# Kernel tuning notes

Hardware: AMD Instinct MI355X
Metric: run time of the kernel (lower is better)

## Reference

```python
import jax, jax.numpy as jnp
import numpy as np

BLOCK_SIZE = 64
SPARSITY_RATIO = 0.5


def _band_mask(seq_len, block_size, sparsity_ratio):
    # Block (i, j) is computed iff max(0, i-w) <= j < min(nb, i+w), w = int(nb*ratio).
    nb = seq_len // block_size
    w = int(nb * sparsity_ratio)
    ib = jnp.arange(nb)
    bm = (ib[None, :] >= ib[:, None] - w) & (ib[None, :] < ib[:, None] + w)  # [nb, nb]
    return jnp.repeat(jnp.repeat(bm, block_size, axis=0), block_size, axis=1)  # [S, S]


def setup_inputs() -> dict:
    key = jax.random.key(0)
    kq, kk, kv = jax.random.split(key, 3)
    B, S, D = 4, 4096, 128
    return {
        "query": jax.random.normal(kq, (B, S, D), dtype=jnp.float32),
        "key": jax.random.normal(kk, (B, S, D), dtype=jnp.float32),
        "value": jax.random.normal(kv, (B, S, D), dtype=jnp.float32),
    }


def reference(query, key, value):
    B, S, D = query.shape
    mask = _band_mask(S, BLOCK_SIZE, SPARSITY_RATIO)  # [S, S] bool
    scores = jnp.einsum('bqd,bkd->bqk', query, key)  # [B, S, S]
    # Outside-band entries stay exactly 0 (NOT -inf) — matches torch.zeros init.
    scores = jnp.where(mask[None, :, :], scores, jnp.zeros((), scores.dtype))
    probs = jax.nn.softmax(scores, axis=-1)
    return jnp.matmul(probs, value)  # [B, S, D]
```

## Files before the change

### kernel.cpp

```cpp
#include <hip/hip_runtime.h>


typedef _Float16 f16;
typedef __attribute__((ext_vector_type(8))) _Float16 f16x8;
typedef __attribute__((ext_vector_type(4))) _Float16 f16x4;
typedef __attribute__((ext_vector_type(4))) float f32x4;
typedef __attribute__((ext_vector_type(8))) short short8;
typedef __attribute__((ext_vector_type(4))) unsigned short u16x4;
typedef __attribute__((ext_vector_type(8))) unsigned short u16x8;

#define MFMA16(a, b, c) __builtin_amdgcn_mfma_f32_16x16x32_f16((a), (b), (c), 0, 0, 0)
#define MFMABF(a, b, c) __builtin_amdgcn_mfma_f32_16x16x32_bf16((a), (b), (c), 0, 0, 0)

#define BATCH 4
#define SEQ   4096
#define DIM   128
#define NB    64
#define WBAND 32
#define LOG2E 1.44269504088896f
#define TSTR  72

#define TILE  16384
#define CHUNKS 8
#define PART_STRIDE 16896

#define KA_OFF 0
#define KB_OFF 16384
#define VA_OFF 32768
#define VB_OFF 49152

#define WAIT0 asm volatile("s_waitcnt vmcnt(0)" ::: "memory")

__device__ __forceinline__ void gl16(const char* g, char* l) {
  __builtin_amdgcn_global_load_lds(
      (const __attribute__((address_space(1))) void*)g,
      (__attribute__((address_space(3))) void*)l, 16, 0, 0);
}

__device__ __forceinline__ unsigned int pk_bf16(float a, float b) {
  unsigned int r;
  asm("v_cvt_pk_bf16_f32 %0, %1, %2" : "=v"(r) : "v"(a), "v"(b));
  return r;
}

__device__ __forceinline__ unsigned short f2bf(float x) {
  unsigned int u = __float_as_uint(x);
  u += 0x7FFFu + ((u >> 16) & 1u);
  return (unsigned short)(u >> 16);
}

__global__ __launch_bounds__(256) void convert_kernel(
    const float* __restrict__ K, const float* __restrict__ V,
    f16* __restrict__ KF, unsigned short* __restrict__ VF,
    float* __restrict__ BS) {
  __shared__ unsigned short T[128 * TSTR];
  const int blk = blockIdx.x;
  const int b = blk >> 6, jb = blk & 63;
  const int s0 = jb * 64;
  const int t = threadIdx.x;

#pragma unroll
  for (int i = 0; i < 8; ++i) {
    int idx = t + i * 256;
    int row = idx >> 5;
    int c4 = (idx & 31) * 4;
    float4 v = *(const float4*)(V + (size_t)(b * SEQ + s0 + row) * DIM + c4);
    T[(c4 + 0) * TSTR + row] = f2bf(v.x);
    T[(c4 + 1) * TSTR + row] = f2bf(v.y);
    T[(c4 + 2) * TSTR + row] = f2bf(v.z);
    T[(c4 + 3) * TSTR + row] = f2bf(v.w);
  }

  char* kt = (char*)KF + (size_t)blk * TILE;
#pragma unroll
  for (int i = 0; i < 4; ++i) {
    int idx = t + i * 256;
    int frag = idx >> 6, lane = idx & 63;
    int ks = frag >> 2, jt = frag & 3;
    int row = jt * 16 + (lane & 15);
    int d0 = ks * 32 + (lane >> 4) * 8;
    const float* src = K + ((size_t)(b * SEQ + s0 + row)) * DIM + d0;
    float4 a = *(const float4*)src;
    float4 d = *(const float4*)(src + 4);
    f16x8 h = {(f16)a.x, (f16)a.y, (f16)a.z, (f16)a.w,
               (f16)d.x, (f16)d.y, (f16)d.z, (f16)d.w};
    *(f16x8*)(kt + idx * 16) = h;
  }
  __syncthreads();

  char* vt = (char*)VF + (size_t)blk * TILE;
#pragma unroll
  for (int i = 0; i < 4; ++i) {
    int idx = t + i * 256;
    int frag = idx >> 6, lane = idx & 63;
    int ks2 = frag >> 3, nt = frag & 7;
    int d = nt * 16 + (lane & 15);
    int k0 = ks2 * 32 + ((lane >> 4) & 3) * 4;
    u16x4 x = *(const u16x4*)(T + d * TSTR + k0);
    u16x4 y = *(const u16x4*)(T + d * TSTR + k0 + 16);
    u16x8 h = {x[0], x[1], x[2], x[3], y[0], y[1], y[2], y[3]};
    *(u16x8*)(vt + idx * 16) = h;
  }

  if (t < 128) {
    float s = 0.f;
    for (int k = 0; k < 64; ++k)
      s += __uint_as_float(((unsigned int)T[t * TSTR + k]) << 16);
    BS[(b * NB + jb) * DIM + t] = s;
  }
}

__global__ __launch_bounds__(256, 2) void attn_kernel(
    const float* __restrict__ Q, const f16* __restrict__ KF,
    const unsigned short* __restrict__ VF, char* __restrict__ PART) {
  __shared__ __align__(16) char smem[65536];

  const int id = blockIdx.x;
  const int lin = (id & 7) * 128 + (id >> 3);
  const int ck = lin & 7;
  const int pair = lin >> 3;
  const int b = pair >> 5, p = pair & 31;

  const int t = threadIdx.x;
  const int w = t >> 6, l = t & 63, lg = l >> 4, ll = l & 15;
  const int half = w >> 1, qh = w & 1;
  const int myib = p * 2 + half;

  const int jloU = max(0, p * 2 - WBAND);
  const int jhiU = min(NB, p * 2 + 1 + WBAND);
  const int lenU = jhiU - jloU;
  const int base = lenU >> 3, rem = lenU & 7;
  const int j0 = jloU + ck * base + min(ck, rem);
  const int nloc = base + (ck < rem ? 1 : 0);
  const int mylo = max(0, myib - WBAND);
  const int myhi = min(NB, myib + WBAND);

  f16x8 qf[2][4];
#pragma unroll
  for (int s = 0; s < 2; ++s) {
    const float* qrow =
        Q + ((size_t)(b * SEQ + myib * 64 + qh * 32 + s * 16 + ll)) * DIM;
#pragma unroll
    for (int ks = 0; ks < 4; ++ks) {
      int d0 = ks * 32 + lg * 8;
      float4 a = *(const float4*)(qrow + d0);
      float4 cc = *(const float4*)(qrow + d0 + 4);
      float vv[8] = {a.x, a.y, a.z, a.w, cc.x, cc.y, cc.z, cc.w};
#pragma unroll
      for (int e = 0; e < 8; ++e) qf[s][ks][e] = (f16)(vv[e] * LOG2E);
    }
  }

  float ell[2] = {0.f, 0.f};
  f32x4 o[2][8];
#pragma unroll
  for (int s = 0; s < 2; ++s)
#pragma unroll
    for (int nt = 0; nt < 8; ++nt) o[s][nt] = (f32x4){0.f, 0.f, 0.f, 0.f};

  auto stage_group = [&](int g) {
    const int jA = j0 + 2 * g;
    {
      const char* kg = (const char*)KF + ((size_t)(b * NB + jA)) * TILE + t * 16;
      const char* vg = (const char*)VF + ((size_t)(b * NB + jA)) * TILE + t * 16;
#pragma unroll
      for (int i = 0; i < 4; ++i) gl16(kg + i * 4096, smem + KA_OFF + t * 16 + i * 4096);
#pragma unroll
      for (int i = 0; i < 4; ++i) gl16(vg + i * 4096, smem + VA_OFF + t * 16 + i * 4096);
    }
    if (2 * g + 1 < nloc) {
      const int jB = jA + 1;
      const char* kg = (const char*)KF + ((size_t)(b * NB + jB)) * TILE + t * 16;
      const char* vg = (const char*)VF + ((size_t)(b * NB + jB)) * TILE + t * 16;
#pragma unroll
      for (int i = 0; i < 4; ++i) gl16(kg + i * 4096, smem + KB_OFF + t * 16 + i * 4096);
#pragma unroll
      for (int i = 0; i < 4; ++i) gl16(vg + i * 4096, smem + VB_OFF + t * 16 + i * 4096);
    }
  };

  auto compute = [&](int j, const char* kb, const char* vb) {
    if (j < mylo || j >= myhi) return;

    f32x4 sacc[2][4];
#pragma unroll
    for (int s = 0; s < 2; ++s)
#pragma unroll
      for (int jt = 0; jt < 4; ++jt) sacc[s][jt] = (f32x4){0.f, 0.f, 0.f, 0.f};

    __builtin_amdgcn_s_setprio(1);
#pragma unroll
    for (int ks = 0; ks < 4; ++ks) {
#pragma unroll
      for (int jt = 0; jt < 4; ++jt) {
        f16x8 kf = *(const f16x8*)(kb + (ks * 4 + jt) * 1024 + l * 16);
        sacc[0][jt] = MFMA16(kf, qf[0][ks], sacc[0][jt]);
        sacc[1][jt] = MFMA16(kf, qf[1][ks], sacc[1][jt]);
      }
    }
    __builtin_amdgcn_s_setprio(0);

    short8 pa[2][2];
#pragma unroll
    for (int s = 0; s < 2; ++s) {
      float rsum = 0.f;
#pragma unroll
      for (int ks2 = 0; ks2 < 2; ++ks2) {
        float pe[8];
#pragma unroll
        for (int u = 0; u < 2; ++u)
#pragma unroll
          for (int r = 0; r < 4; ++r) {
            float p = __builtin_amdgcn_exp2f(sacc[s][ks2 * 2 + u][r]);
            rsum += p;
            pe[u * 4 + r] = p;
          }
        union { unsigned int w[4]; short8 v; } pk;
#pragma unroll
        for (int h2 = 0; h2 < 4; ++h2)
          pk.w[h2] = pk_bf16(pe[h2 * 2], pe[h2 * 2 + 1]);
        pa[s][ks2] = pk.v;
      }
      ell[s] += rsum;
    }

    __builtin_amdgcn_s_setprio(1);
#pragma unroll
    for (int ks2 = 0; ks2 < 2; ++ks2) {
#pragma unroll
      for (int nt = 0; nt < 8; ++nt) {
        short8 vbf = *(const short8*)(vb + (ks2 * 8 + nt) * 1024 + l * 16);
        o[0][nt] = MFMABF(pa[0][ks2], vbf, o[0][nt]);
        o[1][nt] = MFMABF(pa[1][ks2], vbf, o[1][nt]);
      }
    }
    __builtin_amdgcn_s_setprio(0);
  };

  const int ng = (nloc + 1) >> 1;
  stage_group(0);
  for (int g = 0; g < ng; ++g) {
    WAIT0;
    __syncthreads();

    compute(j0 + 2 * g, smem + KA_OFF, smem + VA_OFF);
    if (2 * g + 1 < nloc)
      compute(j0 + 2 * g + 1, smem + KB_OFF, smem + VB_OFF);

    __syncthreads();
    if (g + 1 < ng) stage_group(g + 1);
  }

#pragma unroll
  for (int s = 0; s < 2; ++s) {
    ell[s] += __shfl_xor(ell[s], 16);
    ell[s] += __shfl_xor(ell[s], 32);
  }

  float sb[2][4];
#pragma unroll
  for (int s = 0; s < 2; ++s) {
    float rinv = 1.f / ell[s];
#pragma unroll
    for (int r = 0; r < 4; ++r) sb[s][r] = __shfl(rinv, lg * 4 + r);
  }

  char* pb = PART + ((size_t)((pair * CHUNKS + ck) * 2 + half)) * PART_STRIDE;
#pragma unroll
  for (int s = 0; s < 2; ++s)
#pragma unroll
    for (int g = 0; g < 4; ++g) {
      f16x8 hh;
#pragma unroll
      for (int r = 0; r < 4; ++r) {
        hh[r] = (f16)(o[s][2 * g][r] * sb[s][r]);
        hh[4 + r] = (f16)(o[s][2 * g + 1][r] * sb[s][r]);
      }
      *(f16x8*)(pb + qh * 8192 + ((s * 4 + g) * 64 + l) * 16) = hh;
    }
  if (lg == 0) {
#pragma unroll
    for (int s = 0; s < 2; ++s)
      *(float2*)(pb + 16384 + (qh * 32 + s * 16 + ll) * 8) =
          make_float2(0.f, ell[s]);
  }
}

__global__ __launch_bounds__(256) void merge_kernel(
    const char* __restrict__ PART, const float* __restrict__ BS,
    float* __restrict__ Out) {
  __shared__ float VoutS[DIM];
  __shared__ float mlS[CHUNKS][64][2];

  const int id = blockIdx.x;
  const int lin = (id & 7) * 32 + (id >> 3);
  const int pair = lin >> 1, half = lin & 1;
  const int b = pair >> 5;
  const int ib = (pair & 31) * 2 + half;
  const int t = threadIdx.x;
  const int l = t & 63, lg = (t >> 4) & 3, ll = t & 15;
  const int sub = (t >> 6) & 1, qh = t >> 7;

  const int jlo = max(0, ib - WBAND);
  const int jhi = min(NB, ib + WBAND);
  const float cnt_out = (float)(SEQ - (jhi - jlo) * 64);

  if (t < DIM) {
    float s = 0.f;
    for (int j = 0; j < jlo; ++j) s += BS[(b * NB + j) * DIM + t];
    for (int j = jhi; j < NB; ++j) s += BS[(b * NB + j) * DIM + t];
    VoutS[t] = s;
  }

  const size_t pb0 = ((size_t)(pair * CHUNKS * 2 + half)) * PART_STRIDE;
  for (int i = t; i < CHUNKS * 64; i += 256) {
    int k = i >> 6, row = i & 63;
    *(float2*)&mlS[k][row][0] = *(const float2*)(
        PART + pb0 + (size_t)k * 2 * PART_STRIDE + 16384 + row * 8);
  }
  __syncthreads();

  float aw[4][CHUNKS], inv[4];
#pragma unroll
  for (int r = 0; r < 4; ++r) {
    int row = qh * 32 + sub * 16 + lg * 4 + r;
    float den = cnt_out;
#pragma unroll
    for (int k = 0; k < CHUNKS; ++k) {
      aw[r][k] = mlS[k][row][1];
      den += aw[r][k];
    }
    inv[r] = 1.f / den;
  }

  float acc[8][4];
#pragma unroll
  for (int nt = 0; nt < 8; ++nt)
#pragma unroll
    for (int r = 0; r < 4; ++r) acc[nt][r] = 0.f;

  for (int k = 0; k < CHUNKS; ++k) {
    const char* oc = PART + pb0 + (size_t)k * 2 * PART_STRIDE + qh * 8192;
#pragma unroll
    for (int g = 0; g < 4; ++g) {
      f16x8 h = *(const f16x8*)(oc + ((sub * 4 + g) * 64 + l) * 16);
#pragma unroll
      for (int r = 0; r < 4; ++r) {
        acc[2 * g][r] += aw[r][k] * (float)h[r];
        acc[2 * g + 1][r] += aw[r][k] * (float)h[4 + r];
      }
    }
  }

  const int q0 = ib * 64;
#pragma unroll
  for (int nt = 0; nt < 8; ++nt) {
    int col = nt * 16 + ll;
    float vout = VoutS[col];
#pragma unroll
    for (int r = 0; r < 4; ++r) {
      int row = qh * 32 + sub * 16 + lg * 4 + r;
      Out[((size_t)(b * SEQ + q0 + row)) * DIM + col] =
          (acc[nt][r] + vout) * inv[r];
    }
  }
}

extern "C" void kernel_launch(void* const* d_in, const int* in_sizes, int n_in,
                              void* d_out, int out_size, void* d_ws, size_t ws_size,
                              hipStream_t stream) {
  const float* Q = (const float*)d_in[0];
  const float* K = (const float*)d_in[1];
  const float* V = (const float*)d_in[2];
  float* Out = (float*)d_out;

  char* ws = (char*)d_ws;
  f16* KF = (f16*)ws;
  unsigned short* VF = (unsigned short*)(ws + (size_t)BATCH * NB * TILE);
  float* BS = (float*)(ws + 2 * (size_t)BATCH * NB * TILE);
  char* PART = ws + 2 * (size_t)BATCH * NB * TILE + (size_t)BATCH * NB * DIM * 4;

  convert_kernel<<<dim3(BATCH * NB), 256, 0, stream>>>(K, V, KF, VF, BS);
  attn_kernel<<<dim3(BATCH * NB / 2 * CHUNKS), 256, 0, stream>>>(Q, KF, VF, PART);
  merge_kernel<<<dim3(BATCH * NB), 256, 0, stream>>>(PART, BS, Out);
}
```

Baseline: 58.82 us.

## Load V fragments directly from global into registers, stage only K in LDS

Shrinks shared memory from 64KB to 16KB by staging only one K tile per iteration in LDS. V fragments are loaded straight from global memory into registers at the start of each compute step, so their latency overlaps the QK MFMAs and softmax. The two-tile grouped pipeline is replaced by a single-tile loop with two barriers per tile and no overlap of the K load with compute. The goal is higher occupancy and less LDS traffic, at the cost of more registers, exposed K-load latency and more frequent synchronisation.

```diff
diff --git a/kernel.cpp b/kernel.cpp
--- a/kernel.cpp
+++ b/kernel.cpp
@@ -23,13 +23,6 @@
 #define TILE  16384
 #define CHUNKS 8
 #define PART_STRIDE 16896
-
-#define KA_OFF 0
-#define KB_OFF 16384
-#define VA_OFF 32768
-#define VB_OFF 49152
-
-#define WAIT0 asm volatile("s_waitcnt vmcnt(0)" ::: "memory")
 
 __device__ __forceinline__ void gl16(const char* g, char* l) {
   __builtin_amdgcn_global_load_lds(
@@ -113,7 +106,7 @@
 __global__ __launch_bounds__(256, 2) void attn_kernel(
     const float* __restrict__ Q, const f16* __restrict__ KF,
     const unsigned short* __restrict__ VF, char* __restrict__ PART) {
-  __shared__ __align__(16) char smem[65536];
+  __shared__ __align__(16) char smem[16384];
 
   const int id = blockIdx.x;
   const int lin = (id & 7) * 128 + (id >> 3);
@@ -158,97 +151,86 @@
 #pragma unroll
     for (int nt = 0; nt < 8; ++nt) o[s][nt] = (f32x4){0.f, 0.f, 0.f, 0.f};
 
-  auto stage_group = [&](int g) {
-    const int jA = j0 + 2 * g;
-    {
-      const char* kg = (const char*)KF + ((size_t)(b * NB + jA)) * TILE + t * 16;
-      const char* vg = (const char*)VF + ((size_t)(b * NB + jA)) * TILE + t * 16;
-#pragma unroll
-      for (int i = 0; i < 4; ++i) gl16(kg + i * 4096, smem + KA_OFF + t * 16 + i * 4096);
-#pragma unroll
-      for (int i = 0; i < 4; ++i) gl16(vg + i * 4096, smem + VA_OFF + t * 16 + i * 4096);
-    }
-    if (2 * g + 1 < nloc) {
-      const int jB = jA + 1;
-      const char* kg = (const char*)KF + ((size_t)(b * NB + jB)) * TILE + t * 16;
-      const char* vg = (const char*)VF + ((size_t)(b * NB + jB)) * TILE + t * 16;
-#pragma unroll
-      for (int i = 0; i < 4; ++i) gl16(kg + i * 4096, smem + KB_OFF + t * 16 + i * 4096);
-#pragma unroll
-      for (int i = 0; i < 4; ++i) gl16(vg + i * 4096, smem + VB_OFF + t * 16 + i * 4096);
-    }
+  auto stageK = [&](int jb) {
+    const char* kg = (const char*)KF + ((size_t)(b * NB + jb)) * TILE + t * 16;
+#pragma unroll
+    for (int i = 0; i < 4; ++i) gl16(kg + i * 4096, smem + t * 16 + i * 4096);
   };
 
-  auto compute = [&](int j, const char* kb, const char* vb) {
-    if (j < mylo || j >= myhi) return;
-
-    f32x4 sacc[2][4];
-#pragma unroll
-    for (int s = 0; s < 2; ++s)
-#pragma unroll
-      for (int jt = 0; jt < 4; ++jt) sacc[s][jt] = (f32x4){0.f, 0.f, 0.f, 0.f};
-
-    __builtin_amdgcn_s_setprio(1);
-#pragma unroll
-    for (int ks = 0; ks < 4; ++ks) {
-#pragma unroll
-      for (int jt = 0; jt < 4; ++jt) {
-        f16x8 kf = *(const f16x8*)(kb + (ks * 4 + jt) * 1024 + l * 16);
-        sacc[0][jt] = MFMA16(kf, qf[0][ks], sacc[0][jt]);
-        sacc[1][jt] = MFMA16(kf, qf[1][ks], sacc[1][jt]);
-      }
-    }
-    __builtin_amdgcn_s_setprio(0);
-
-    short8 pa[2][2];
-#pragma unroll
-    for (int s = 0; s < 2; ++s) {
-      float rsum = 0.f;
-#pragma unroll
-      for (int ks2 = 0; ks2 < 2; ++ks2) {
-        float pe[8];
-#pragma unroll
-        for (int u = 0; u < 2; ++u)
-#pragma unroll
-          for (int r = 0; r < 4; ++r) {
-            float p = __builtin_amdgcn_exp2f(sacc[s][ks2 * 2 + u][r]);
-            rsum += p;
-            pe[u * 4 + r] = p;
-          }
-        union { unsigned int w[4]; short8 v; } pk;
-#pragma unroll
-        for (int h2 = 0; h2 < 4; ++h2)
-          pk.w[h2] = pk_bf16(pe[h2 * 2], pe[h2 * 2 + 1]);
-        pa[s][ks2] = pk.v;
-      }
-      ell[s] += rsum;
-    }
-
-    __builtin_amdgcn_s_setprio(1);
-#pragma unroll
-    for (int ks2 = 0; ks2 < 2; ++ks2) {
+  stageK(j0);
+  __syncthreads();
+
+  for (int tt = 0; tt < nloc; ++tt) {
+    const int j = j0 + tt;
+    if (j >= mylo && j < myhi) {
+      const char* vt =
+          (const char*)VF + ((size_t)(b * NB + j)) * TILE + (size_t)l * 16;
+      short8 vr0[8], vr1[8];
+#pragma unroll
+      for (int nt = 0; nt < 8; ++nt) vr0[nt] = *(const short8*)(vt + nt * 1024);
+#pragma unroll
+      for (int nt = 0; nt < 8; ++nt)
+        vr1[nt] = *(const short8*)(vt + (8 + nt) * 1024);
+
+      f32x4 sacc[2][4];
+#pragma unroll
+      for (int s = 0; s < 2; ++s)
+#pragma unroll
+        for (int jt = 0; jt < 4; ++jt) sacc[s][jt] = (f32x4){0.f, 0.f, 0.f, 0.f};
+
+      __builtin_amdgcn_s_setprio(1);
+#pragma unroll
+      for (int ks = 0; ks < 4; ++ks) {
+#pragma unroll
+        for (int jt = 0; jt < 4; ++jt) {
+          f16x8 kf = *(const f16x8*)(smem + (ks * 4 + jt) * 1024 + l * 16);
+          sacc[0][jt] = MFMA16(kf, qf[0][ks], sacc[0][jt]);
+          sacc[1][jt] = MFMA16(kf, qf[1][ks], sacc[1][jt]);
+        }
+      }
+      __builtin_amdgcn_s_setprio(0);
+
+      short8 pa[2][2];
+#pragma unroll
+      for (int s = 0; s < 2; ++s) {
+        float rsum = 0.f;
+#pragma unroll
+        for (int ks2 = 0; ks2 < 2; ++ks2) {
+          float pe[8];
+#pragma unroll
+          for (int u = 0; u < 2; ++u)
+#pragma unroll
+            for (int r = 0; r < 4; ++r) {
+              float pv = __builtin_amdgcn_exp2f(sacc[s][ks2 * 2 + u][r]);
+              rsum += pv;
+              pe[u * 4 + r] = pv;
+            }
+          union { unsigned int w2[4]; short8 v; } pk;
+#pragma unroll
+          for (int h2 = 0; h2 < 4; ++h2)
+            pk.w2[h2] = pk_bf16(pe[h2 * 2], pe[h2 * 2 + 1]);
+          pa[s][ks2] = pk.v;
+        }
+        ell[s] += rsum;
+      }
+
+      __builtin_amdgcn_s_setprio(1);
 #pragma unroll
       for (int nt = 0; nt < 8; ++nt) {
-        short8 vbf = *(const short8*)(vb + (ks2 * 8 + nt) * 1024 + l * 16);
-        o[0][nt] = MFMABF(pa[0][ks2], vbf, o[0][nt]);
-        o[1][nt] = MFMABF(pa[1][ks2], vbf, o[1][nt]);
-      }
-    }
-    __builtin_amdgcn_s_setprio(0);
-  };
-
-  const int ng = (nloc + 1) >> 1;
-  stage_group(0);
-  for (int g = 0; g < ng; ++g) {
-    WAIT0;
+        o[0][nt] = MFMABF(pa[0][0], vr0[nt], o[0][nt]);
+        o[1][nt] = MFMABF(pa[1][0], vr0[nt], o[1][nt]);
+      }
+#pragma unroll
+      for (int nt = 0; nt < 8; ++nt) {
+        o[0][nt] = MFMABF(pa[0][1], vr1[nt], o[0][nt]);
+        o[1][nt] = MFMABF(pa[1][1], vr1[nt], o[1][nt]);
+      }
+      __builtin_amdgcn_s_setprio(0);
+    }
+
     __syncthreads();
-
-    compute(j0 + 2 * g, smem + KA_OFF, smem + VA_OFF);
-    if (2 * g + 1 < nloc)
-      compute(j0 + 2 * g + 1, smem + KB_OFF, smem + VB_OFF);
-
+    if (tt + 1 < nloc) stageK(j0 + tt + 1);
     __syncthreads();
-    if (g + 1 < ng) stage_group(g + 1);
   }
 
 #pragma unroll
```

Measured after the change: 60.59 us. 1.03x slower.
